# Performance work log

Hardware: AMD Instinct MI355X
Metric: run time of the kernel (lower is better)

Reference implementation:

```python
import jax, jax.numpy as jnp
import numpy as np

N_NODES = 50000
N_EDGES = 800000
IN_DIM, HID, N_CLS = 128, 128, 64


def setup_inputs() -> dict:
    key = jax.random.key(0)
    ks = jax.random.split(key, 10)
    x = jax.random.normal(ks[0], (N_NODES, IN_DIM), dtype=jnp.float32)
    src = jax.random.randint(ks[1], (N_EDGES,), 0, N_NODES, dtype=jnp.int32)
    dst = jax.random.randint(ks[2], (N_EDGES,), 0, N_NODES, dtype=jnp.int32)
    def lin(k, fi, fo):
        s = 1.0 / np.sqrt(fi)
        return jax.random.uniform(k, (fi, fo), jnp.float32, -s, s)
    # layer dims: 128->128, 128->128, 128->64 (num_layers=2 -> 3 SAGEConv layers)
    params = {
        'W_self0': lin(ks[3], IN_DIM, HID), 'W_neigh0': lin(ks[4], IN_DIM, HID),
        'b0': jnp.zeros((HID,), jnp.float32),
        'W_self1': lin(ks[5], HID, HID), 'W_neigh1': lin(ks[6], HID, HID),
        'b1': jnp.zeros((HID,), jnp.float32),
        'W_self2': lin(ks[7], HID, N_CLS), 'W_neigh2': lin(ks[8], HID, N_CLS),
        'b2': jnp.zeros((N_CLS,), jnp.float32),
    }
    return {'x': x, 'src': src, 'dst': dst, **params}


def _sage_layer(h, src, dst, W_self, W_neigh, b):
    # mean aggregator: gather source features, segment-sum into dst, divide by in-degree
    msg = h[src]                                                   # [E, d]
    agg = jax.ops.segment_sum(msg, dst, num_segments=N_NODES)      # [N, d]
    deg = jax.ops.segment_sum(jnp.ones((src.shape[0],), h.dtype), dst,
                              num_segments=N_NODES)
    h_neigh = agg / jnp.maximum(deg, 1.0)[:, None]
    return h @ W_self + h_neigh @ W_neigh + b


def reference(x, src, dst, W_self0, W_neigh0, b0, W_self1, W_neigh1, b1,
              W_self2, W_neigh2, b2):
    h = _sage_layer(x, src, dst, W_self0, W_neigh0, b0)
    h = jax.nn.relu(h)
    h = _sage_layer(h, src, dst, W_self1, W_neigh1, b1)
    h = jax.nn.relu(h)
    h = _sage_layer(h, src, dst, W_self2, W_neigh2, b2)
    return h
```

## Files before the change

kernel.cpp:

```cpp
#include <hip/hip_runtime.h>
#include <hip/hip_bf16.h>


#define NFEAT 128
#define SLOTS 64
#define BSH 9
#define BNODES (1 << BSH)
#define MAXBK 100
#define LCAP 64
#define LSH 6
#define MAXTB 256

typedef __attribute__((ext_vector_type(8))) short short8;
typedef __attribute__((ext_vector_type(4))) float floatx4;

__device__ __forceinline__ float bf_lo(unsigned u) { return __uint_as_float(u << 16); }
__device__ __forceinline__ float bf_hi(unsigned u) { return __uint_as_float(u & 0xffff0000u); }
__device__ __forceinline__ ushort f2bf(float f) {
    __hip_bfloat16 h = __float2bfloat16(f);
    return *(ushort*)&h;
}
__device__ __forceinline__ unsigned pack2(float a, float b) {
    return (unsigned)f2bf(a) | ((unsigned)f2bf(b) << 16);
}


__global__ __launch_bounds__(256) void k_p1(
    const int* __restrict__ dst, const int* __restrict__ src,
    unsigned* __restrict__ gbuf, int* __restrict__ lcnt_g,
    unsigned* __restrict__ spill, int* __restrict__ spill_cnt,
    int E, int nbk, int tb, int epb,
    const float* __restrict__ Ws0, const float* __restrict__ Wn0,
    const float* __restrict__ Ws1, const float* __restrict__ Wn1,
    const float* __restrict__ Ws2, const float* __restrict__ Wn2,
    ushort* __restrict__ Wt0, ushort* __restrict__ Wt1, ushort* __restrict__ Wt2) {
    int b = blockIdx.x, t = threadIdx.x;
    if (b < tb) {
        __shared__ unsigned lists[MAXBK * LCAP];
        __shared__ int lcnt[MAXBK];
        for (int i = t; i < MAXBK; i += 256) lcnt[i] = 0;
        __syncthreads();

        int tile0 = b * epb;
        for (int off = t * 4; off < epb; off += 1024) {
            int base = tile0 + off;
            if (base + 4 <= E) {
                int4 d4 = *(const int4*)(dst + base);
                int4 s4 = *(const int4*)(src + base);
                int dd[4] = {d4.x, d4.y, d4.z, d4.w};
                int ss[4] = {s4.x, s4.y, s4.z, s4.w};
#pragma unroll
                for (int j = 0; j < 4; ++j) {
                    int bkt = dd[j] >> BSH;
                    unsigned pk = ((unsigned)ss[j] << 16) | (unsigned)dd[j];
                    int pos = atomicAdd(&lcnt[bkt], 1);
                    if (pos < LCAP) {
                        lists[(bkt << LSH) + pos] = pk;
                    } else {
                        int g = atomicAdd(spill_cnt, 1);
                        spill[g] = pk;
                    }
                }
            } else {
                for (int e = base; e < E && e < base + 4; ++e) {
                    int d = dst[e];
                    int bkt = d >> BSH;
                    unsigned pk = ((unsigned)src[e] << 16) | (unsigned)d;
                    int pos = atomicAdd(&lcnt[bkt], 1);
                    if (pos < LCAP) {
                        lists[(bkt << LSH) + pos] = pk;
                    } else {
                        int g = atomicAdd(spill_cnt, 1);
                        spill[g] = pk;
                    }
                }
            }
        }
        __syncthreads();

        int lane = t & 63, wid = t >> 6;
        for (int bk = wid; bk < nbk; bk += 4) {
            int c = lcnt[bk];
            if (c > LCAP) c = LCAP;
            if (lane == 0) lcnt_g[bk * tb + b] = c;
            unsigned* seg = gbuf + (((size_t)bk * tb + b) << LSH);
            for (int i = lane; i < c; i += 64) seg[i] = lists[(bk << LSH) + i];
        }
    } else {
        int idx = (b - tb) * 256 + t;
        if (idx < 32768) {
            int n = idx >> 8, k = idx & 255;
            Wt0[idx] = f2bf(k < 128 ? Ws0[k * 128 + n] : Wn0[(k - 128) * 128 + n]);
        } else if (idx < 65536) {
            int l = idx - 32768, n = l >> 8, k = l & 255;
            Wt1[l] = f2bf(k < 128 ? Ws1[k * 128 + n] : Wn1[(k - 128) * 128 + n]);
        } else if (idx < 81920) {
            int l = idx - 65536, n = l >> 8, k = l & 255;
            Wt2[l] = f2bf(k < 128 ? Ws2[k * 64 + n] : Wn2[(k - 128) * 64 + n]);
        }
    }
}


__global__ __launch_bounds__(256) void k_p2(
    const unsigned* __restrict__ gbuf, const int* __restrict__ lcnt_g,
    const unsigned* __restrict__ spill, const int* __restrict__ spill_cnt,
    int* __restrict__ deg, ushort* __restrict__ csr, int NN, int nbk, int tb,
    const float* __restrict__ X, ushort* __restrict__ X16, int n2) {
    int b = blockIdx.x, t = threadIdx.x;
    if (b < nbk) {
        __shared__ int cnt[BNODES];
        __shared__ int scnt[MAXTB];
        for (int i = t; i < BNODES; i += 256) cnt[i] = 0;
        for (int i = t; i < tb; i += 256) scnt[i] = lcnt_g[b * tb + i];
        __syncthreads();
        int n0 = b << BSH;
        const unsigned* bp = gbuf + (((size_t)b * tb) << LSH);
        int total = tb << LSH;
        for (int j0 = t * 4; j0 < total; j0 += 1024) {
            int blk = j0 >> LSH;
            int c = scnt[blk];
            int idx0 = j0 & (LCAP - 1);
            uint4 v = *(const uint4*)(bp + j0);
            unsigned pp[4] = {v.x, v.y, v.z, v.w};
#pragma unroll
            for (int k = 0; k < 4; ++k) {
                if (idx0 + k < c) {
                    unsigned p = pp[k];
                    int d = (int)(p & 0xFFFFu);
                    int s = (int)(p >> 16);
                    int r = atomicAdd(&cnt[d - n0], 1);
                    if (r < SLOTS) csr[(d << 6) + r] = (ushort)s;
                }
            }
        }
        int ns = *spill_cnt;
        for (int j = t; j < ns; j += 256) {
            unsigned p = spill[j];
            int d = (int)(p & 0xFFFFu);
            if ((d >> BSH) == b) {
                int s = (int)(p >> 16);
                int r = atomicAdd(&cnt[d - n0], 1);
                if (r < SLOTS) csr[(d << 6) + r] = (ushort)s;
            }
        }
        __syncthreads();
        for (int i = t; i < BNODES; i += 256) {
            int n = n0 + i;
            if (n < NN) deg[n] = cnt[i];
        }
    } else {
        int i = (b - nbk) * 256 + t;
        if (i < n2) {
            float2 v = ((const float2*)X)[i];
            ((unsigned*)X16)[i] = pack2(v.x, v.y);
        }
    }
}


template <int FEAT, int MODE>
__device__ __forceinline__ void agg_body(int vbid, int nb, int t,
    const ushort* __restrict__ H, const int* __restrict__ deg,
    const ushort* __restrict__ csr, void* __restrict__ outp, int NN) {
    constexpr int LPR = FEAT / 8;
    constexpr int EPG = 64 / LPR;
    constexpr int NS = 8;
    int lane = t & 63, wid = t >> 6;
    int sub = lane / LPR, fl = lane % LPR;
    int wstr = nb * 4;
    int node = vbid * 4 + wid;

    int d_cur = 0;
    int s_cur[NS];
    if (node < NN) {
        d_cur = deg[node];
        const ushort* slot = csr + (node << 6);
#pragma unroll
        for (int k = 0; k < NS; ++k) s_cur[k] = slot[k * EPG + sub];
    }

    while (node < NN) {
        int nnode = node + wstr;
        int d_nxt = 0;
        int s_nxt[NS];
        if (nnode < NN) {
            d_nxt = deg[nnode];
            const ushort* slot2 = csr + (nnode << 6);
#pragma unroll
            for (int k = 0; k < NS; ++k) s_nxt[k] = slot2[k * EPG + sub];
        }

        int dd = d_cur;
        int d = (dd < SLOTS) ? dd : SLOTS;
        float acc[8] = {};
        uint4 v[NS];
#pragma unroll
        for (int k = 0; k < NS; ++k) {
            int e = k * EPG + sub;
            v[k] = make_uint4(0, 0, 0, 0);
            if (e < d) v[k] = *(const uint4*)(H + (size_t)s_cur[k] * FEAT + fl * 8);
        }
#pragma unroll
        for (int k = 0; k < NS; ++k) {
            acc[0] += bf_lo(v[k].x); acc[1] += bf_hi(v[k].x);
            acc[2] += bf_lo(v[k].y); acc[3] += bf_hi(v[k].y);
            acc[4] += bf_lo(v[k].z); acc[5] += bf_hi(v[k].z);
            acc[6] += bf_lo(v[k].w); acc[7] += bf_hi(v[k].w);
        }
        if constexpr (NS * EPG < SLOTS) {
            if (d > NS * EPG) {
                const ushort* slot = csr + (node << 6);
                for (int e = NS * EPG + sub; e < d; e += EPG) {
                    int r = slot[e];
                    uint4 vv = *(const uint4*)(H + (size_t)r * FEAT + fl * 8);
                    acc[0] += bf_lo(vv.x); acc[1] += bf_hi(vv.x);
                    acc[2] += bf_lo(vv.y); acc[3] += bf_hi(vv.y);
                    acc[4] += bf_lo(vv.z); acc[5] += bf_hi(vv.z);
                    acc[6] += bf_lo(vv.w); acc[7] += bf_hi(vv.w);
                }
            }
        }
#pragma unroll
        for (int off = LPR; off < 64; off <<= 1)
#pragma unroll
            for (int i = 0; i < 8; ++i) acc[i] += __shfl_xor(acc[i], off, 64);
        if (sub == 0) {
            float inv = (dd > 0) ? 1.0f / (float)dd : 0.0f;
            if constexpr (MODE == 0) {
                unsigned u[4];
#pragma unroll
                for (int i = 0; i < 4; ++i)
                    u[i] = pack2(acc[2 * i] * inv, acc[2 * i + 1] * inv);
                *(uint4*)((ushort*)outp + (size_t)node * FEAT + fl * 8) =
                    make_uint4(u[0], u[1], u[2], u[3]);
            } else {
                float* O = (float*)outp;
                size_t b = (size_t)node * FEAT + fl * 8;
#pragma unroll
                for (int i = 0; i < 8; ++i) O[b + i] += acc[i] * inv;
            }
        }
        node = nnode;
        d_cur = d_nxt;
#pragma unroll
        for (int k = 0; k < NS; ++k) s_cur[k] = s_nxt[k];
    }
}

__global__ __launch_bounds__(256) void k_agg128(
    const ushort* __restrict__ H, const int* __restrict__ deg,
    const ushort* __restrict__ csr, void* __restrict__ outp, int NN) {
    agg_body<128, 0>(blockIdx.x, gridDim.x, threadIdx.x, H, deg, csr, outp, NN);
}

__global__ __launch_bounds__(256) void k_aggacc(
    const ushort* __restrict__ G2, const int* __restrict__ deg,
    const ushort* __restrict__ csr, float* __restrict__ out, int NN) {
    agg_body<64, 2>(blockIdx.x, gridDim.x, threadIdx.x, G2, deg, csr, out, NN);
}


template <int BM, int BN, int NKB, bool SPLIT, bool OUT_BF16>
__device__ __forceinline__ void gemm_body(int bid, int t,
    const ushort* __restrict__ Hs, const ushort* __restrict__ Ag,
    const ushort* __restrict__ Wt, int ldw, const float* __restrict__ bias,
    void* __restrict__ Cout, int M, int relu) {
    constexpr int NW = BN / 64;
    constexpr int NTHR = 2 * NW * 64;
    constexpr int MT = BM / 32;
    constexpr int LDA = 40;
    __shared__ ushort Asl[BM * LDA];
    __shared__ ushort Bsl[BN * LDA];

    int lane = t & 63;
    int wid = t >> 6;
    int wm = wid & 1, wn = wid >> 1;
    int l15 = lane & 15, quad = lane >> 4;
    int m0 = bid * BM;

    floatx4 acc[MT][4] = {};

    for (int kb = 0; kb < NKB; ++kb) {
        const ushort* Asrc;
        int kOff;
        if constexpr (SPLIT) {
            Asrc = (kb < NKB / 2) ? Hs : Ag;
            kOff = (kb & (NKB / 2 - 1)) * 32;
        } else {
            Asrc = Hs;
            kOff = kb * 32;
        }
        __syncthreads();
#pragma unroll
        for (int id = t; id < BM * 4; id += NTHR) {
            int r = id >> 2, p = id & 3;
            uint4 v = make_uint4(0, 0, 0, 0);
            if (m0 + r < M) v = *(const uint4*)(Asrc + (size_t)(m0 + r) * NFEAT + kOff + p * 8);
            *(uint4*)(&Asl[r * LDA + p * 8]) = v;
        }
#pragma unroll
        for (int id = t; id < BN * 4; id += NTHR) {
            int r = id >> 2, p = id & 3;
            uint4 v = *(const uint4*)(Wt + (size_t)r * ldw + kb * 32 + p * 8);
            *(uint4*)(&Bsl[r * LDA + p * 8]) = v;
        }
        __syncthreads();

        short8 a[MT], b[4];
#pragma unroll
        for (int mt = 0; mt < MT; ++mt)
            a[mt] = *(const short8*)(&Asl[(wm * (MT * 16) + mt * 16 + l15) * LDA + quad * 8]);
#pragma unroll
        for (int nt = 0; nt < 4; ++nt)
            b[nt] = *(const short8*)(&Bsl[(wn * 64 + nt * 16 + l15) * LDA + quad * 8]);
#pragma unroll
        for (int mt = 0; mt < MT; ++mt)
#pragma unroll
            for (int nt = 0; nt < 4; ++nt)
                acc[mt][nt] = __builtin_amdgcn_mfma_f32_16x16x32_bf16(a[mt], b[nt], acc[mt][nt], 0, 0, 0);
    }

#pragma unroll
    for (int mt = 0; mt < MT; ++mt) {
        int mbase = m0 + wm * (MT * 16) + mt * 16 + quad * 4;
#pragma unroll
        for (int nt = 0; nt < 4; ++nt) {
            int col = wn * 64 + nt * 16 + l15;
            float bv = bias ? bias[col] : 0.0f;
#pragma unroll
            for (int r = 0; r < 4; ++r) {
                int m = mbase + r;
                if (m < M) {
                    float v = acc[mt][nt][r] + bv;
                    if (relu) v = fmaxf(v, 0.f);
                    if constexpr (OUT_BF16) {
                        ((unsigned short*)Cout)[(size_t)m * BN + col] = f2bf(v);
                    } else {
                        ((float*)Cout)[(size_t)m * BN + col] = v;
                    }
                }
            }
        }
    }
}

__global__ __launch_bounds__(256) void k_gemm(
    const ushort* __restrict__ Hs, const ushort* __restrict__ Ag,
    const ushort* __restrict__ Wt, const float* __restrict__ bias,
    ushort* __restrict__ Hout, int M) {
    gemm_body<64, 128, 8, true, true>(blockIdx.x, threadIdx.x,
                                      Hs, Ag, Wt, 256, bias, Hout, M, 1);
}

__global__ __launch_bounds__(128) void k_d7(
    const ushort* __restrict__ Hb, const ushort* __restrict__ Wt2,
    const float* __restrict__ b2, ushort* __restrict__ G2,
    float* __restrict__ out, int M, int pb) {
    if ((int)blockIdx.x < pb)
        gemm_body<64, 64, 4, false, true>(blockIdx.x, threadIdx.x,
                                          Hb, nullptr, Wt2 + 128, 256, nullptr, G2, M, 0);
    else
        gemm_body<64, 64, 4, false, false>(blockIdx.x - pb, threadIdx.x,
                                           Hb, nullptr, Wt2, 256, b2, out, M, 0);
}


static inline size_t align_up(size_t x) { return (x + 255) & ~(size_t)255; }

extern "C" void kernel_launch(void* const* d_in, const int* in_sizes, int n_in,
                              void* d_out, int out_size, void* d_ws, size_t ws_size,
                              hipStream_t stream) {
    const float* x   = (const float*)d_in[0];
    const int*   src = (const int*)d_in[1];
    const int*   dst = (const int*)d_in[2];
    const float* Ws0 = (const float*)d_in[3];
    const float* Wn0 = (const float*)d_in[4];
    const float* b0  = (const float*)d_in[5];
    const float* Ws1 = (const float*)d_in[6];
    const float* Wn1 = (const float*)d_in[7];
    const float* b1  = (const float*)d_in[8];
    const float* Ws2 = (const float*)d_in[9];
    const float* Wn2 = (const float*)d_in[10];
    const float* b2  = (const float*)d_in[11];
    float* out = (float*)d_out;

    const int NN = in_sizes[0] / NFEAT;
    const int E  = in_sizes[1];

    char* w = (char*)d_ws;
    ushort* X16  = (ushort*)w; w += align_up((size_t)NN * NFEAT * 2);
    ushort* Ha   = (ushort*)w; w += align_up((size_t)NN * NFEAT * 2);
    ushort* Hb   = (ushort*)w; w += align_up((size_t)NN * NFEAT * 2);
    ushort* AGG  = (ushort*)w; w += align_up((size_t)NN * NFEAT * 2);
    ushort* Wt0  = (ushort*)w; w += align_up((size_t)128 * 256 * 2);
    ushort* Wt1  = (ushort*)w; w += align_up((size_t)128 * 256 * 2);
    ushort* Wt2  = (ushort*)w; w += align_up((size_t)64 * 256 * 2);
    int* deg     = (int*)w;    w += align_up((size_t)NN * 4);
    ushort* csr  = (ushort*)w; w += align_up((size_t)NN * SLOTS * 2);

    int epb = 4096;
    int tb = (E + epb - 1) / epb;
    if (tb > MAXTB) { epb = ((E + MAXTB - 1) / MAXTB + 1023) & ~(size_t)1023; tb = (E + epb - 1) / epb; }
    const int nbk = (NN + BNODES - 1) >> BSH;

    unsigned* gbuf   = (unsigned*)Ha;
    int* lcnt_g      = (int*)Hb;
    int* spill_cnt   = lcnt_g + nbk * tb;
    unsigned* spill  = (unsigned*)AGG;
    ushort* G2       = X16;

    hipMemsetAsync(spill_cnt, 0, 4, stream);

    const int n2   = NN * NFEAT / 2;
    const int cvtb = (n2 + 255) / 256;
    const int wb   = (81920 + 255) / 256;
    const int gm   = (NN + 63) / 64;
    const int agb  = 2048;

    k_p1<<<tb + wb, 256, 0, stream>>>(
        dst, src, gbuf, lcnt_g, spill, spill_cnt, E, nbk, tb, epb,
        Ws0, Wn0, Ws1, Wn1, Ws2, Wn2, Wt0, Wt1, Wt2);

    k_p2<<<nbk + cvtb, 256, 0, stream>>>(
        gbuf, lcnt_g, spill, spill_cnt, deg, csr, NN, nbk, tb, x, X16, n2);

    k_agg128<<<agb, 256, 0, stream>>>(X16, deg, csr, AGG, NN);
    k_gemm<<<gm, 256, 0, stream>>>(X16, AGG, Wt0, b0, Ha, NN);

    k_agg128<<<agb, 256, 0, stream>>>(Ha, deg, csr, AGG, NN);
    k_gemm<<<gm, 256, 0, stream>>>(Ha, AGG, Wt1, b1, Hb, NN);

    k_d7<<<gm * 2, 128, 0, stream>>>(Hb, Wt2, b2, G2, out, NN, gm);
    k_aggacc<<<agb, 256, 0, stream>>>(G2, deg, csr, out, NN);
}
```

Measured before the change: 240.7 us.

## Fuse neighbor aggregation into layer GEMMs and fold final projection into layer 1

Each of the first two SAGE layers now does its mean aggregation inside the GEMM block, one 64-row tile at a time. The aggregated rows go into shared memory, so the AGG buffer round trip and one launch per layer go away. Layer 1 also keeps its ReLU output in shared memory and immediately runs the final 128->64 self and neighbor projections, which removes the separate k_d7 launch and the Hb write and read. In exchange, gather parallelism is tied to only about 782 blocks, and per-block shared memory use goes up, which may cut occupancy and gather latency hiding. The final 64-wide aggregation also drops its spill loop for degrees above 64 slots, which matches the cap the CSR already imposes.

```diff
diff --git a/kernel.cpp b/kernel.cpp
--- a/kernel.cpp
+++ b/kernel.cpp
@@ -159,17 +159,245 @@
 }
 
 
-template <int FEAT, int MODE>
-__device__ __forceinline__ void agg_body(int vbid, int nb, int t,
+template <bool FUSE_D7>
+__device__ __forceinline__ void layer_body(
+    int bid, int t,
     const ushort* __restrict__ H, const int* __restrict__ deg,
-    const ushort* __restrict__ csr, void* __restrict__ outp, int NN) {
-    constexpr int LPR = FEAT / 8;
-    constexpr int EPG = 64 / LPR;
-    constexpr int NS = 8;
+    const ushort* __restrict__ csr, const ushort* __restrict__ Wt,
+    const float* __restrict__ bias, ushort* __restrict__ Hout,
+    const ushort* __restrict__ Wt2, const float* __restrict__ b2,
+    ushort* __restrict__ G2, float* __restrict__ out, int M) {
+    constexpr int LDA = 40;
+    constexpr int LDG = 136;
+    __shared__ ushort Asl[64 * LDA];
+    __shared__ ushort Bsl[128 * LDA];
+    __shared__ ushort Agl[64 * LDG];
+
+    int lane = t & 63, wid = t >> 6;
+    int m0 = bid * 64;
+
+    {
+        int sub = lane >> 4, fl = lane & 15;
+        int r0 = wid * 16;
+        int dd_c = 0;
+        int sx_c[8];
+        {
+            int node = m0 + r0;
+            if (node < M) {
+                dd_c = deg[node];
+                const ushort* sl = csr + (node << 6);
+#pragma unroll
+                for (int k = 0; k < 8; ++k) sx_c[k] = sl[(k << 2) + sub];
+            }
+        }
+        for (int i = 0; i < 16; ++i) {
+            int dd_n = 0;
+            int sx_n[8];
+            if (i < 15) {
+                int nn = m0 + r0 + i + 1;
+                if (nn < M) {
+                    dd_n = deg[nn];
+                    const ushort* sl = csr + (nn << 6);
+#pragma unroll
+                    for (int k = 0; k < 8; ++k) sx_n[k] = sl[(k << 2) + sub];
+                }
+            }
+            int dd = dd_c;
+            int d = (dd < SLOTS) ? dd : SLOTS;
+            float acc[8] = {};
+            uint4 v[8];
+#pragma unroll
+            for (int k = 0; k < 8; ++k) {
+                v[k] = make_uint4(0, 0, 0, 0);
+                if ((k << 2) + sub < d)
+                    v[k] = *(const uint4*)(H + (size_t)sx_c[k] * NFEAT + fl * 8);
+            }
+#pragma unroll
+            for (int k = 0; k < 8; ++k) {
+                acc[0] += bf_lo(v[k].x); acc[1] += bf_hi(v[k].x);
+                acc[2] += bf_lo(v[k].y); acc[3] += bf_hi(v[k].y);
+                acc[4] += bf_lo(v[k].z); acc[5] += bf_hi(v[k].z);
+                acc[6] += bf_lo(v[k].w); acc[7] += bf_hi(v[k].w);
+            }
+            if (d > 32) {
+                const ushort* sl = csr + ((m0 + r0 + i) << 6);
+                for (int e = 32 + sub; e < d; e += 4) {
+                    int s = sl[e];
+                    uint4 vv = *(const uint4*)(H + (size_t)s * NFEAT + fl * 8);
+                    acc[0] += bf_lo(vv.x); acc[1] += bf_hi(vv.x);
+                    acc[2] += bf_lo(vv.y); acc[3] += bf_hi(vv.y);
+                    acc[4] += bf_lo(vv.z); acc[5] += bf_hi(vv.z);
+                    acc[6] += bf_lo(vv.w); acc[7] += bf_hi(vv.w);
+                }
+            }
+#pragma unroll
+            for (int off = 16; off < 64; off <<= 1)
+#pragma unroll
+                for (int q = 0; q < 8; ++q) acc[q] += __shfl_xor(acc[q], off, 64);
+            if (sub == 0) {
+                float inv = (dd > 0) ? 1.0f / (float)dd : 0.0f;
+                unsigned u[4];
+#pragma unroll
+                for (int q = 0; q < 4; ++q)
+                    u[q] = pack2(acc[2 * q] * inv, acc[2 * q + 1] * inv);
+                *(uint4*)(&Agl[(r0 + i) * LDG + fl * 8]) = make_uint4(u[0], u[1], u[2], u[3]);
+            }
+            dd_c = dd_n;
+#pragma unroll
+            for (int k = 0; k < 8; ++k) sx_c[k] = sx_n[k];
+        }
+    }
+
+    int wm = wid & 1, wn = wid >> 1;
+    int l15 = lane & 15, quad = lane >> 4;
+    floatx4 acc[2][4] = {};
+
+    for (int kb = 0; kb < 8; ++kb) {
+        int kOff = (kb & 3) * 32;
+        __syncthreads();
+        if (kb < 4) {
+#pragma unroll
+            for (int id = t; id < 64 * 4; id += 256) {
+                int r = id >> 2, p = id & 3;
+                uint4 v = make_uint4(0, 0, 0, 0);
+                if (m0 + r < M) v = *(const uint4*)(H + (size_t)(m0 + r) * NFEAT + kOff + p * 8);
+                *(uint4*)(&Asl[r * LDA + p * 8]) = v;
+            }
+        }
+#pragma unroll
+        for (int id = t; id < 128 * 4; id += 256) {
+            int r = id >> 2, p = id & 3;
+            uint4 v = *(const uint4*)(Wt + (size_t)r * 256 + kb * 32 + p * 8);
+            *(uint4*)(&Bsl[r * LDA + p * 8]) = v;
+        }
+        __syncthreads();
+
+        short8 a[2], b[4];
+#pragma unroll
+        for (int mt = 0; mt < 2; ++mt) {
+            int row = wm * 32 + mt * 16 + l15;
+            if (kb < 4)
+                a[mt] = *(const short8*)(&Asl[row * LDA + quad * 8]);
+            else
+                a[mt] = *(const short8*)(&Agl[row * LDG + kOff + quad * 8]);
+        }
+#pragma unroll
+        for (int nt = 0; nt < 4; ++nt)
+            b[nt] = *(const short8*)(&Bsl[(wn * 64 + nt * 16 + l15) * LDA + quad * 8]);
+#pragma unroll
+        for (int mt = 0; mt < 2; ++mt)
+#pragma unroll
+            for (int nt = 0; nt < 4; ++nt)
+                acc[mt][nt] = __builtin_amdgcn_mfma_f32_16x16x32_bf16(a[mt], b[nt], acc[mt][nt], 0, 0, 0);
+    }
+
+    if constexpr (!FUSE_D7) {
+#pragma unroll
+        for (int mt = 0; mt < 2; ++mt) {
+            int mbase = m0 + wm * 32 + mt * 16 + quad * 4;
+#pragma unroll
+            for (int nt = 0; nt < 4; ++nt) {
+                int col = wn * 64 + nt * 16 + l15;
+                float bv = bias[col];
+#pragma unroll
+                for (int r = 0; r < 4; ++r) {
+                    int m = mbase + r;
+                    if (m < M) {
+                        float v = acc[mt][nt][r] + bv;
+                        v = fmaxf(v, 0.f);
+                        Hout[(size_t)m * NFEAT + col] = f2bf(v);
+                    }
+                }
+            }
+        }
+    } else {
+        __syncthreads();
+#pragma unroll
+        for (int mt = 0; mt < 2; ++mt) {
+            int rbase = wm * 32 + mt * 16 + quad * 4;
+#pragma unroll
+            for (int nt = 0; nt < 4; ++nt) {
+                int col = wn * 64 + nt * 16 + l15;
+                float bv = bias[col];
+#pragma unroll
+                for (int r = 0; r < 4; ++r) {
+                    float v = acc[mt][nt][r] + bv;
+                    v = fmaxf(v, 0.f);
+                    Agl[(rbase + r) * LDG + col] = f2bf(v);
+                }
+            }
+        }
+        __syncthreads();
+
+        floatx4 accS[4] = {};
+        floatx4 accP[4] = {};
+#pragma unroll
+        for (int half = 0; half < 2; ++half) {
+#pragma unroll
+            for (int kb = 0; kb < 4; ++kb) {
+                __syncthreads();
+#pragma unroll
+                for (int id = t; id < 64 * 4; id += 256) {
+                    int r = id >> 2, p = id & 3;
+                    uint4 v = *(const uint4*)(Wt2 + (size_t)r * 256 + half * 128 + kb * 32 + p * 8);
+                    *(uint4*)(&Bsl[r * LDA + p * 8]) = v;
+                }
+                __syncthreads();
+                short8 a = *(const short8*)(&Agl[(wid * 16 + l15) * LDG + kb * 32 + quad * 8]);
+#pragma unroll
+                for (int nt = 0; nt < 4; ++nt) {
+                    short8 b = *(const short8*)(&Bsl[(nt * 16 + l15) * LDA + quad * 8]);
+                    if (half == 0)
+                        accS[nt] = __builtin_amdgcn_mfma_f32_16x16x32_bf16(a, b, accS[nt], 0, 0, 0);
+                    else
+                        accP[nt] = __builtin_amdgcn_mfma_f32_16x16x32_bf16(a, b, accP[nt], 0, 0, 0);
+                }
+            }
+        }
+#pragma unroll
+        for (int nt = 0; nt < 4; ++nt) {
+            int col = nt * 16 + l15;
+            float bv = b2[col];
+#pragma unroll
+            for (int r = 0; r < 4; ++r) {
+                int m = m0 + wid * 16 + quad * 4 + r;
+                if (m < M) {
+                    out[(size_t)m * 64 + col] = accS[nt][r] + bv;
+                    G2[(size_t)m * 64 + col] = f2bf(accP[nt][r]);
+                }
+            }
+        }
+    }
+}
+
+__global__ __launch_bounds__(256) void k_layer0(
+    const ushort* __restrict__ H, const int* __restrict__ deg,
+    const ushort* __restrict__ csr, const ushort* __restrict__ Wt,
+    const float* __restrict__ bias, ushort* __restrict__ Hout, int M) {
+    layer_body<false>(blockIdx.x, threadIdx.x, H, deg, csr, Wt, bias, Hout,
+                      nullptr, nullptr, nullptr, nullptr, M);
+}
+
+__global__ __launch_bounds__(256) void k_layer1(
+    const ushort* __restrict__ H, const int* __restrict__ deg,
+    const ushort* __restrict__ csr, const ushort* __restrict__ Wt,
+    const float* __restrict__ bias,
+    const ushort* __restrict__ Wt2, const float* __restrict__ b2,
+    ushort* __restrict__ G2, float* __restrict__ out, int M) {
+    layer_body<true>(blockIdx.x, threadIdx.x, H, deg, csr, Wt, bias, nullptr,
+                     Wt2, b2, G2, out, M);
+}
+
+
+__global__ __launch_bounds__(256) void k_aggacc(
+    const ushort* __restrict__ G2, const int* __restrict__ deg,
+    const ushort* __restrict__ csr, float* __restrict__ out, int NN) {
+    constexpr int LPR = 8, EPG = 8, NS = 8;
+    int t = threadIdx.x;
     int lane = t & 63, wid = t >> 6;
     int sub = lane / LPR, fl = lane % LPR;
-    int wstr = nb * 4;
-    int node = vbid * 4 + wid;
+    int wstr = gridDim.x * 4;
+    int node = blockIdx.x * 4 + wid;
 
     int d_cur = 0;
     int s_cur[NS];
@@ -199,7 +427,7 @@
         for (int k = 0; k < NS; ++k) {
             int e = k * EPG + sub;
             v[k] = make_uint4(0, 0, 0, 0);
-            if (e < d) v[k] = *(const uint4*)(H + (size_t)s_cur[k] * FEAT + fl * 8);
+            if (e < d) v[k] = *(const uint4*)(G2 + (size_t)s_cur[k] * 64 + fl * 8);
         }
 #pragma unroll
         for (int k = 0; k < NS; ++k) {
@@ -208,161 +436,21 @@
             acc[4] += bf_lo(v[k].z); acc[5] += bf_hi(v[k].z);
             acc[6] += bf_lo(v[k].w); acc[7] += bf_hi(v[k].w);
         }
-        if constexpr (NS * EPG < SLOTS) {
-            if (d > NS * EPG) {
-                const ushort* slot = csr + (node << 6);
-                for (int e = NS * EPG + sub; e < d; e += EPG) {
-                    int r = slot[e];
-                    uint4 vv = *(const uint4*)(H + (size_t)r * FEAT + fl * 8);
-                    acc[0] += bf_lo(vv.x); acc[1] += bf_hi(vv.x);
-                    acc[2] += bf_lo(vv.y); acc[3] += bf_hi(vv.y);
-                    acc[4] += bf_lo(vv.z); acc[5] += bf_hi(vv.z);
-                    acc[6] += bf_lo(vv.w); acc[7] += bf_hi(vv.w);
-                }
-            }
-        }
 #pragma unroll
         for (int off = LPR; off < 64; off <<= 1)
 #pragma unroll
             for (int i = 0; i < 8; ++i) acc[i] += __shfl_xor(acc[i], off, 64);
         if (sub == 0) {
             float inv = (dd > 0) ? 1.0f / (float)dd : 0.0f;
-            if constexpr (MODE == 0) {
-                unsigned u[4];
-#pragma unroll
-                for (int i = 0; i < 4; ++i)
-                    u[i] = pack2(acc[2 * i] * inv, acc[2 * i + 1] * inv);
-                *(uint4*)((ushort*)outp + (size_t)node * FEAT + fl * 8) =
-                    make_uint4(u[0], u[1], u[2], u[3]);
-            } else {
-                float* O = (float*)outp;
-                size_t b = (size_t)node * FEAT + fl * 8;
-#pragma unroll
-                for (int i = 0; i < 8; ++i) O[b + i] += acc[i] * inv;
-            }
+            size_t b = (size_t)node * 64 + fl * 8;
+#pragma unroll
+            for (int i = 0; i < 8; ++i) out[b + i] += acc[i] * inv;
         }
         node = nnode;
         d_cur = d_nxt;
 #pragma unroll
         for (int k = 0; k < NS; ++k) s_cur[k] = s_nxt[k];
     }
-}
-
-__global__ __launch_bounds__(256) void k_agg128(
-    const ushort* __restrict__ H, const int* __restrict__ deg,
-    const ushort* __restrict__ csr, void* __restrict__ outp, int NN) {
-    agg_body<128, 0>(blockIdx.x, gridDim.x, threadIdx.x, H, deg, csr, outp, NN);
-}
-
-__global__ __launch_bounds__(256) void k_aggacc(
-    const ushort* __restrict__ G2, const int* __restrict__ deg,
-    const ushort* __restrict__ csr, float* __restrict__ out, int NN) {
-    agg_body<64, 2>(blockIdx.x, gridDim.x, threadIdx.x, G2, deg, csr, out, NN);
-}
-
-
-template <int BM, int BN, int NKB, bool SPLIT, bool OUT_BF16>
-__device__ __forceinline__ void gemm_body(int bid, int t,
-    const ushort* __restrict__ Hs, const ushort* __restrict__ Ag,
-    const ushort* __restrict__ Wt, int ldw, const float* __restrict__ bias,
-    void* __restrict__ Cout, int M, int relu) {
-    constexpr int NW = BN / 64;
-    constexpr int NTHR = 2 * NW * 64;
-    constexpr int MT = BM / 32;
-    constexpr int LDA = 40;
-    __shared__ ushort Asl[BM * LDA];
-    __shared__ ushort Bsl[BN * LDA];
-
-    int lane = t & 63;
-    int wid = t >> 6;
-    int wm = wid & 1, wn = wid >> 1;
-    int l15 = lane & 15, quad = lane >> 4;
-    int m0 = bid * BM;
-
-    floatx4 acc[MT][4] = {};
-
-    for (int kb = 0; kb < NKB; ++kb) {
-        const ushort* Asrc;
-        int kOff;
-        if constexpr (SPLIT) {
-            Asrc = (kb < NKB / 2) ? Hs : Ag;
-            kOff = (kb & (NKB / 2 - 1)) * 32;
-        } else {
-            Asrc = Hs;
-            kOff = kb * 32;
-        }
-        __syncthreads();
-#pragma unroll
-        for (int id = t; id < BM * 4; id += NTHR) {
-            int r = id >> 2, p = id & 3;
-            uint4 v = make_uint4(0, 0, 0, 0);
-            if (m0 + r < M) v = *(const uint4*)(Asrc + (size_t)(m0 + r) * NFEAT + kOff + p * 8);
-            *(uint4*)(&Asl[r * LDA + p * 8]) = v;
-        }
-#pragma unroll
-        for (int id = t; id < BN * 4; id += NTHR) {
-            int r = id >> 2, p = id & 3;
-            uint4 v = *(const uint4*)(Wt + (size_t)r * ldw + kb * 32 + p * 8);
-            *(uint4*)(&Bsl[r * LDA + p * 8]) = v;
-        }
-        __syncthreads();
-
-        short8 a[MT], b[4];
-#pragma unroll
-        for (int mt = 0; mt < MT; ++mt)
-            a[mt] = *(const short8*)(&Asl[(wm * (MT * 16) + mt * 16 + l15) * LDA + quad * 8]);
-#pragma unroll
-        for (int nt = 0; nt < 4; ++nt)
-            b[nt] = *(const short8*)(&Bsl[(wn * 64 + nt * 16 + l15) * LDA + quad * 8]);
-#pragma unroll
-        for (int mt = 0; mt < MT; ++mt)
-#pragma unroll
-            for (int nt = 0; nt < 4; ++nt)
-                acc[mt][nt] = __builtin_amdgcn_mfma_f32_16x16x32_bf16(a[mt], b[nt], acc[mt][nt], 0, 0, 0);
-    }
-
-#pragma unroll
-    for (int mt = 0; mt < MT; ++mt) {
-        int mbase = m0 + wm * (MT * 16) + mt * 16 + quad * 4;
-#pragma unroll
-        for (int nt = 0; nt < 4; ++nt) {
-            int col = wn * 64 + nt * 16 + l15;
-            float bv = bias ? bias[col] : 0.0f;
-#pragma unroll
-            for (int r = 0; r < 4; ++r) {
-                int m = mbase + r;
-                if (m < M) {
-                    float v = acc[mt][nt][r] + bv;
-                    if (relu) v = fmaxf(v, 0.f);
-                    if constexpr (OUT_BF16) {
-                        ((unsigned short*)Cout)[(size_t)m * BN + col] = f2bf(v);
-                    } else {
-                        ((float*)Cout)[(size_t)m * BN + col] = v;
-                    }
-                }
-            }
-        }
-    }
-}
-
-__global__ __launch_bounds__(256) void k_gemm(
-    const ushort* __restrict__ Hs, const ushort* __restrict__ Ag,
-    const ushort* __restrict__ Wt, const float* __restrict__ bias,
-    ushort* __restrict__ Hout, int M) {
-    gemm_body<64, 128, 8, true, true>(blockIdx.x, threadIdx.x,
-                                      Hs, Ag, Wt, 256, bias, Hout, M, 1);
-}
-
-__global__ __launch_bounds__(128) void k_d7(
-    const ushort* __restrict__ Hb, const ushort* __restrict__ Wt2,
-    const float* __restrict__ b2, ushort* __restrict__ G2,
-    float* __restrict__ out, int M, int pb) {
-    if ((int)blockIdx.x < pb)
-        gemm_body<64, 64, 4, false, true>(blockIdx.x, threadIdx.x,
-                                          Hb, nullptr, Wt2 + 128, 256, nullptr, G2, M, 0);
-    else
-        gemm_body<64, 64, 4, false, false>(blockIdx.x - pb, threadIdx.x,
-                                           Hb, nullptr, Wt2, 256, b2, out, M, 0);
 }
 
 
@@ -425,12 +513,9 @@
     k_p2<<<nbk + cvtb, 256, 0, stream>>>(
         gbuf, lcnt_g, spill, spill_cnt, deg, csr, NN, nbk, tb, x, X16, n2);
 
-    k_agg128<<<agb, 256, 0, stream>>>(X16, deg, csr, AGG, NN);
-    k_gemm<<<gm, 256, 0, stream>>>(X16, AGG, Wt0, b0, Ha, NN);
-
-    k_agg128<<<agb, 256, 0, stream>>>(Ha, deg, csr, AGG, NN);
-    k_gemm<<<gm, 256, 0, stream>>>(Ha, AGG, Wt1, b1, Hb, NN);
-
-    k_d7<<<gm * 2, 128, 0, stream>>>(Hb, Wt2, b2, G2, out, NN, gm);
+    k_layer0<<<gm, 256, 0, stream>>>(X16, deg, csr, Wt0, b0, Ha, NN);
+
+    k_layer1<<<gm, 256, 0, stream>>>(Ha, deg, csr, Wt1, b1, Wt2, b2, G2, out, NN);
+
     k_aggacc<<<agb, 256, 0, stream>>>(G2, deg, csr, out, NN);
 }
```

Measured after the change: 265.9 us. 10.5% more time.

## Fuse layer-2 projection GEMM into layer-1 GEMM epilogue via shared memory

Applied to the files above, without the earlier changes.

The layer-1 GEMM epilogue now writes its ReLU'd bf16 tile into shared memory and immediately multiplies it by both halves of the layer-2 weights. It emits the fp32 self term plus bias and the bf16 neighbour projection directly. This removes the Hb round trip through global memory and one kernel launch. In exchange the block uses more LDS and runs a second serial GEMM phase, which may reduce occupancy.

```diff
diff --git a/kernel.cpp b/kernel.cpp
--- a/kernel.cpp
+++ b/kernel.cpp
@@ -261,11 +261,13 @@
 }
 
 
-template <int BM, int BN, int NKB, bool SPLIT, bool OUT_BF16>
+template <int BM, int BN, int NKB, bool SPLIT, bool OUT_BF16, bool FUSE_D7>
 __device__ __forceinline__ void gemm_body(int bid, int t,
     const ushort* __restrict__ Hs, const ushort* __restrict__ Ag,
     const ushort* __restrict__ Wt, int ldw, const float* __restrict__ bias,
-    void* __restrict__ Cout, int M, int relu) {
+    void* __restrict__ Cout, int M, int relu,
+    const ushort* __restrict__ Wt2, const float* __restrict__ b2,
+    ushort* __restrict__ G2, float* __restrict__ outF) {
     constexpr int NW = BN / 64;
     constexpr int NTHR = 2 * NW * 64;
     constexpr int MT = BM / 32;
@@ -321,24 +323,83 @@
                 acc[mt][nt] = __builtin_amdgcn_mfma_f32_16x16x32_bf16(a[mt], b[nt], acc[mt][nt], 0, 0, 0);
     }
 
-#pragma unroll
-    for (int mt = 0; mt < MT; ++mt) {
-        int mbase = m0 + wm * (MT * 16) + mt * 16 + quad * 4;
+    if constexpr (!FUSE_D7) {
+#pragma unroll
+        for (int mt = 0; mt < MT; ++mt) {
+            int mbase = m0 + wm * (MT * 16) + mt * 16 + quad * 4;
+#pragma unroll
+            for (int nt = 0; nt < 4; ++nt) {
+                int col = wn * 64 + nt * 16 + l15;
+                float bv = bias ? bias[col] : 0.0f;
+#pragma unroll
+                for (int r = 0; r < 4; ++r) {
+                    int m = mbase + r;
+                    if (m < M) {
+                        float v = acc[mt][nt][r] + bv;
+                        if (relu) v = fmaxf(v, 0.f);
+                        if constexpr (OUT_BF16) {
+                            ((unsigned short*)Cout)[(size_t)m * BN + col] = f2bf(v);
+                        } else {
+                            ((float*)Cout)[(size_t)m * BN + col] = v;
+                        }
+                    }
+                }
+            }
+        }
+    } else {
+        constexpr int LDG = 136;
+        __shared__ ushort Hbl[64 * LDG];
+#pragma unroll
+        for (int mt = 0; mt < MT; ++mt) {
+            int rbase = wm * (MT * 16) + mt * 16 + quad * 4;
+#pragma unroll
+            for (int nt = 0; nt < 4; ++nt) {
+                int col = wn * 64 + nt * 16 + l15;
+                float bv = bias[col];
+#pragma unroll
+                for (int r = 0; r < 4; ++r) {
+                    float v = acc[mt][nt][r] + bv;
+                    v = fmaxf(v, 0.f);
+                    Hbl[(rbase + r) * LDG + col] = f2bf(v);
+                }
+            }
+        }
+
+        floatx4 accS[4] = {};
+        floatx4 accP[4] = {};
+#pragma unroll
+        for (int half = 0; half < 2; ++half) {
+#pragma unroll
+            for (int kb = 0; kb < 4; ++kb) {
+                __syncthreads();
+#pragma unroll
+                for (int id = t; id < 64 * 4; id += NTHR) {
+                    int r = id >> 2, p = id & 3;
+                    uint4 v = *(const uint4*)(Wt2 + (size_t)r * 256 + half * 128 + kb * 32 + p * 8);
+                    *(uint4*)(&Bsl[r * LDA + p * 8]) = v;
+                }
+                __syncthreads();
+                short8 a = *(const short8*)(&Hbl[(wid * 16 + l15) * LDG + kb * 32 + quad * 8]);
+#pragma unroll
+                for (int nt = 0; nt < 4; ++nt) {
+                    short8 b = *(const short8*)(&Bsl[(nt * 16 + l15) * LDA + quad * 8]);
+                    if (half == 0)
+                        accS[nt] = __builtin_amdgcn_mfma_f32_16x16x32_bf16(a, b, accS[nt], 0, 0, 0);
+                    else
+                        accP[nt] = __builtin_amdgcn_mfma_f32_16x16x32_bf16(a, b, accP[nt], 0, 0, 0);
+                }
+            }
+        }
 #pragma unroll
         for (int nt = 0; nt < 4; ++nt) {
-            int col = wn * 64 + nt * 16 + l15;
-            float bv = bias ? bias[col] : 0.0f;
+            int col = nt * 16 + l15;
+            float bv = b2[col];
 #pragma unroll
             for (int r = 0; r < 4; ++r) {
-                int m = mbase + r;
+                int m = m0 + wid * 16 + quad * 4 + r;
                 if (m < M) {
-                    float v = acc[mt][nt][r] + bv;
-                    if (relu) v = fmaxf(v, 0.f);
-                    if constexpr (OUT_BF16) {
-                        ((unsigned short*)Cout)[(size_t)m * BN + col] = f2bf(v);
-                    } else {
-                        ((float*)Cout)[(size_t)m * BN + col] = v;
-                    }
+                    outF[(size_t)m * 64 + col] = accS[nt][r] + bv;
+                    G2[(size_t)m * 64 + col] = f2bf(accP[nt][r]);
                 }
             }
         }
@@ -349,20 +410,17 @@
     const ushort* __restrict__ Hs, const ushort* __restrict__ Ag,
     const ushort* __restrict__ Wt, const float* __restrict__ bias,
     ushort* __restrict__ Hout, int M) {
-    gemm_body<64, 128, 8, true, true>(blockIdx.x, threadIdx.x,
-                                      Hs, Ag, Wt, 256, bias, Hout, M, 1);
-}
-
-__global__ __launch_bounds__(128) void k_d7(
-    const ushort* __restrict__ Hb, const ushort* __restrict__ Wt2,
-    const float* __restrict__ b2, ushort* __restrict__ G2,
-    float* __restrict__ out, int M, int pb) {
-    if ((int)blockIdx.x < pb)
-        gemm_body<64, 64, 4, false, true>(blockIdx.x, threadIdx.x,
-                                          Hb, nullptr, Wt2 + 128, 256, nullptr, G2, M, 0);
-    else
-        gemm_body<64, 64, 4, false, false>(blockIdx.x - pb, threadIdx.x,
-                                           Hb, nullptr, Wt2, 256, b2, out, M, 0);
+    gemm_body<64, 128, 8, true, true, false>(blockIdx.x, threadIdx.x,
+        Hs, Ag, Wt, 256, bias, Hout, M, 1, nullptr, nullptr, nullptr, nullptr);
+}
+
+__global__ __launch_bounds__(256) void k_gemm1d7(
+    const ushort* __restrict__ Hs, const ushort* __restrict__ Ag,
+    const ushort* __restrict__ Wt, const float* __restrict__ bias,
+    const ushort* __restrict__ Wt2, const float* __restrict__ b2,
+    ushort* __restrict__ G2, float* __restrict__ out, int M) {
+    gemm_body<64, 128, 8, true, true, true>(blockIdx.x, threadIdx.x,
+        Hs, Ag, Wt, 256, bias, nullptr, M, 1, Wt2, b2, G2, out);
 }
 
 
@@ -429,8 +487,7 @@
     k_gemm<<<gm, 256, 0, stream>>>(X16, AGG, Wt0, b0, Ha, NN);
 
     k_agg128<<<agb, 256, 0, stream>>>(Ha, deg, csr, AGG, NN);
-    k_gemm<<<gm, 256, 0, stream>>>(Ha, AGG, Wt1, b1, Hb, NN);
-
-    k_d7<<<gm * 2, 128, 0, stream>>>(Hb, Wt2, b2, G2, out, NN, gm);
+    k_gemm1d7<<<gm, 256, 0, stream>>>(Ha, AGG, Wt1, b1, Wt2, b2, G2, out, NN);
+
     k_aggacc<<<agb, 256, 0, stream>>>(G2, deg, csr, out, NN);
 }
```

Result: faster. 233.8 us (-2.9%).
